# Performance work log

Hardware: AMD Instinct MI355X
Metric: run time of the kernel (lower is better)

Reference implementation:

```python
import jax, jax.numpy as jnp
import numpy as np
import math

B, C_IN, H, W_DIM, D_DIM = 2, 128, 24, 24, 24
D_MODEL, N_HEAD, N_LAYERS, D_FF = 256, 8, 4, 512
D_K = D_MODEL // N_HEAD
EPS = 1e-6


def setup_inputs() -> dict:
    key = jax.random.key(0)
    ks = jax.random.split(key, 16)
    s = 0.02
    inp = {
        "x": jax.random.normal(ks[0], (B, C_IN, H, W_DIM, D_DIM), jnp.float32),
        # 1x1x1 Conv3d W_x: weight [out, in], bias [out]
        "Wx_w": jax.random.normal(ks[1], (D_MODEL, C_IN), jnp.float32) * s,
        "Wx_b": jnp.zeros((D_MODEL,), jnp.float32),
        # per-layer attention projections (stacked over layers)
        "Wq": jax.random.normal(ks[2], (N_LAYERS, D_MODEL, D_MODEL), jnp.float32) * s,
        "bq": jnp.zeros((N_LAYERS, D_MODEL), jnp.float32),
        "Wk": jax.random.normal(ks[3], (N_LAYERS, D_MODEL, D_MODEL), jnp.float32) * s,
        "bk": jnp.zeros((N_LAYERS, D_MODEL), jnp.float32),
        "Wv": jax.random.normal(ks[4], (N_LAYERS, D_MODEL, D_MODEL), jnp.float32) * s,
        "bv": jnp.zeros((N_LAYERS, D_MODEL), jnp.float32),
        "Wo": jax.random.normal(ks[5], (N_LAYERS, D_MODEL, D_MODEL), jnp.float32) * s,
        "bo": jnp.zeros((N_LAYERS, D_MODEL), jnp.float32),
        # layer norms
        "ln1_g": jnp.ones((N_LAYERS, D_MODEL), jnp.float32),
        "ln1_b": jnp.zeros((N_LAYERS, D_MODEL), jnp.float32),
        "ln2_g": jnp.ones((N_LAYERS, D_MODEL), jnp.float32),
        "ln2_b": jnp.zeros((N_LAYERS, D_MODEL), jnp.float32),
        # FFN
        "ffn_w1": jax.random.normal(ks[6], (N_LAYERS, D_MODEL, D_FF), jnp.float32) * s,
        "ffn_b1": jnp.zeros((N_LAYERS, D_FF), jnp.float32),
        "ffn_w2": jax.random.normal(ks[7], (N_LAYERS, D_FF, D_MODEL), jnp.float32) * s,
        "ffn_b2": jnp.zeros((N_LAYERS, D_MODEL), jnp.float32),
        # depthwise 3x3x3 conv positional encoder (groups = D_MODEL)
        "pos_w": jax.random.normal(ks[8], (N_LAYERS, D_MODEL, 1, 3, 3, 3), jnp.float32) * s,
        "pos_b": jnp.zeros((N_LAYERS, D_MODEL), jnp.float32),
    }
    return inp


def _layer_norm(t, g, b):
    mu = jnp.mean(t, axis=-1, keepdims=True)
    var = jnp.var(t, axis=-1, keepdims=True)
    return (t - mu) * jax.lax.rsqrt(var + EPS) * g + b


def reference(x, Wx_w, Wx_b, Wq, bq, Wk, bk, Wv, bv, Wo, bo,
              ln1_g, ln1_b, ln2_g, ln2_b,
              ffn_w1, ffn_b1, ffn_w2, ffn_b2, pos_w, pos_b):
    b = x.shape[0]
    # 1x1x1 conv projection W_x + ReLU (is_up=False path)
    x = jnp.einsum('bchwd,oc->bohwd', x, Wx_w) + Wx_b[None, :, None, None, None]
    x = jax.nn.relu(x)

    inv_sqrt_dk = 1.0 / math.sqrt(D_K)

    for i in range(N_LAYERS):
        # flatten spatial -> tokens: [b, n, d_model]
        t = jnp.transpose(x.reshape(b, D_MODEL, -1), (0, 2, 1))
        n = t.shape[1]

        def heads(y):  # [b,n,d] -> [b,h,n,dk]
            return jnp.transpose(y.reshape(b, n, N_HEAD, D_K), (0, 2, 1, 3))

        q = heads(t @ Wq[i] + bq[i])
        k = heads(t @ Wk[i] + bk[i])
        v = heads(t @ Wv[i] + bv[i])

        # linear attention: softmax over feature dim for q, token dim for k
        q = jax.nn.softmax(q, axis=-1) * inv_sqrt_dk
        k = jax.nn.softmax(k, axis=-2)
        ctx = jnp.einsum('bhnd,bhne->bhde', k, v)     # [b,h,dk,dk]
        o = jnp.einsum('bhnd,bhde->bhne', q, ctx)      # [b,h,n,dk]
        o = jnp.transpose(o, (0, 2, 1, 3)).reshape(b, n, D_MODEL)
        o = o @ Wo[i] + bo[i]

        t = _layer_norm(t + o, ln1_g[i], ln1_b[i])
        f = jax.nn.gelu(t @ ffn_w1[i] + ffn_b1[i], approximate=False) @ ffn_w2[i] + ffn_b2[i]
        t = _layer_norm(t + f, ln2_g[i], ln2_b[i])

        # back to volume and depthwise conv positional embedding
        x = jnp.transpose(t, (0, 2, 1)).reshape(b, D_MODEL, H, W_DIM, D_DIM)
        pos = jax.lax.conv_general_dilated(
            x, pos_w[i], window_strides=(1, 1, 1), padding='SAME',
            dimension_numbers=('NCDHW', 'OIDHW', 'NCDHW'),
            feature_group_count=D_MODEL,
        ) + pos_b[i][None, :, None, None, None]
        x = x + pos
    return x
```

## Files before the change

### kernel.cpp

```cpp
#include <hip/hip_runtime.h>
#include <math.h>

#define NTOK 13824
#define MTOT 27648
#define BATCH 2
#define CIN 128
#define DMODEL 256
#define NHEAD 8
#define NLAYERS 4
#define DFF 512
#define NSPLIT 27
#define KVHALF ((size_t)BATCH * 256 * NTOK)

typedef float f32x4 __attribute__((ext_vector_type(4)));
typedef __bf16 bf16x8 __attribute__((ext_vector_type(8)));
typedef __attribute__((address_space(1))) void gvoid;
typedef __attribute__((address_space(3))) void lvoid;

#define GLDS16(g, l) __builtin_amdgcn_global_load_lds((gvoid*)(g), (lvoid*)(l), 16, 0, 0)

__device__ __forceinline__ unsigned short f2bf(float f) {
    unsigned u = __float_as_uint(f);
    return (unsigned short)((u + 0x7FFFu + ((u >> 16) & 1u)) >> 16);
}
__device__ __forceinline__ float bf2f(unsigned short h) {
    return __uint_as_float(((unsigned)h) << 16);
}

template<int ACT, int OUTM>
__global__ __launch_bounds__(256) void gemm_bf16(
    const unsigned short* __restrict__ A, int lda,
    const unsigned short* __restrict__ Bt, int ldb,
    const float* __restrict__ bias,
    float* __restrict__ Cf, unsigned short* __restrict__ Cb,
    int ldc, int K, long sA, long sB, long sC)
{
    A  += (size_t)blockIdx.z * sA;
    Bt += (size_t)blockIdx.z * sB;
    if (OUTM == 2) Cf += (size_t)blockIdx.z * sC;
    Cb += (size_t)blockIdx.z * sC;

    __shared__ __attribute__((aligned(16))) unsigned short As[4096];
    __shared__ __attribute__((aligned(16))) unsigned short Bs[4096];
    const int t    = threadIdx.x;
    const int lane = t & 63;
    const int wave = t >> 6;
    const int wm = wave & 1, wn = wave >> 1;
    const int m0 = blockIdx.x * 128, n0 = blockIdx.y * 128;

    const int r0   = t >> 2;
    const int koff = (t & 3) * 8;
    const unsigned short* ga0 = A  + (size_t)(m0 + r0)      * lda + koff;
    const unsigned short* ga1 = A  + (size_t)(m0 + r0 + 64) * lda + koff;
    const unsigned short* gb0 = Bt + (size_t)(n0 + r0)      * ldb + koff;
    const unsigned short* gb1 = Bt + (size_t)(n0 + r0 + 64) * ldb + koff;
    unsigned short* la0 = As + t * 8;
    unsigned short* la1 = As + t * 8 + 2048;
    unsigned short* lb0 = Bs + t * 8;
    unsigned short* lb1 = Bs + t * 8 + 2048;

    f32x4 acc[4][4];
    #pragma unroll
    for (int i = 0; i < 4; ++i)
        #pragma unroll
        for (int j = 0; j < 4; ++j) acc[i][j] = (f32x4)0.0f;

    const int fm = lane & 15;
    const int fq = (lane >> 4) * 8;
    const int arow = (wm * 64 + fm) * 32 + fq;
    const int brow = (wn * 64 + fm) * 32 + fq;

    for (int k0 = 0; k0 < K; k0 += 32) {
        GLDS16(ga0 + k0, la0);
        GLDS16(ga1 + k0, la1);
        GLDS16(gb0 + k0, lb0);
        GLDS16(gb1 + k0, lb1);
        __syncthreads();
        bf16x8 af[4], bg[4];
        #pragma unroll
        for (int i = 0; i < 4; ++i) af[i] = *(const bf16x8*)(As + arow + i * 512);
        #pragma unroll
        for (int j = 0; j < 4; ++j) bg[j] = *(const bf16x8*)(Bs + brow + j * 512);
        #pragma unroll
        for (int i = 0; i < 4; ++i)
            #pragma unroll
            for (int j = 0; j < 4; ++j)
                acc[i][j] = __builtin_amdgcn_mfma_f32_16x16x32_bf16(
                    af[i], bg[j], acc[i][j], 0, 0, 0);
        __syncthreads();
    }

    const int cb  = n0 + wn * 64 + fm;
    const int rbs = m0 + wm * 64 + (lane >> 4) * 4;
    #pragma unroll
    for (int j = 0; j < 4; ++j) {
        const int n = cb + j * 16;
        const float bv = bias[n];
        #pragma unroll
        for (int i = 0; i < 4; ++i) {
            #pragma unroll
            for (int r = 0; r < 4; ++r) {
                float v = acc[i][j][r] + bv;
                if (ACT == 1) v = fmaxf(v, 0.0f);
                if (ACT == 2) v = 0.5f * v * (1.0f + erff(v * 0.7071067811865476f));
                const size_t off = (size_t)(rbs + i * 16 + r) * ldc + n;
                if (OUTM == 2) Cf[off] = v;
                Cb[off] = f2bf(v);
            }
        }
    }
}

#define CW_QKV  786432
#define CW_O   1048576
#define CW_1   1572864
#define CW_2   2097152
#define CW_X   2129920
#define CW_B   2132992
__global__ __launch_bounds__(256) void conv_weights(
    const float* __restrict__ Wq, const float* __restrict__ Wk,
    const float* __restrict__ Wv, const float* __restrict__ Wo,
    const float* __restrict__ fw1, const float* __restrict__ fw2,
    const float* __restrict__ Wx_w,
    const float* __restrict__ bq, const float* __restrict__ bk,
    const float* __restrict__ bv,
    unsigned short* __restrict__ wqkv_t, unsigned short* __restrict__ wo_t,
    unsigned short* __restrict__ w1_t, unsigned short* __restrict__ w2_t,
    unsigned short* __restrict__ wx_bf, float* __restrict__ bqkv)
{
    const int e = blockIdx.x * 256 + threadIdx.x;
    if (e < CW_QKV) {
        const int i = e / 196608, r = e % 196608;
        const int n = r / 256, k = r % 256;
        const float* src = (n < 256) ? Wq : (n < 512) ? Wk : Wv;
        wqkv_t[e] = f2bf(src[((size_t)i * 256 + k) * 256 + (n & 255)]);
    } else if (e < CW_O) {
        const int r = e - CW_QKV;
        const int i = r / 65536, rr = r % 65536, n = rr / 256, k = rr % 256;
        wo_t[r] = f2bf(Wo[((size_t)i * 256 + k) * 256 + n]);
    } else if (e < CW_1) {
        const int r = e - CW_O;
        const int i = r / 131072, rr = r % 131072, n = rr / 256, k = rr % 256;
        w1_t[r] = f2bf(fw1[((size_t)i * 256 + k) * 512 + n]);
    } else if (e < CW_2) {
        const int r = e - CW_1;
        const int i = r / 131072, rr = r % 131072, n = rr / 512, k = rr % 512;
        w2_t[r] = f2bf(fw2[((size_t)i * 512 + k) * 256 + n]);
    } else if (e < CW_X) {
        const int r = e - CW_2;
        wx_bf[r] = f2bf(Wx_w[r]);
    } else if (e < CW_B) {
        const int r = e - CW_X;
        const int i = r / 768, j = r % 768;
        const float v = (j < 256) ? bq[i * 256 + j]
                      : (j < 512) ? bk[i * 256 + j - 256]
                                  : bv[i * 256 + j - 512];
        bqkv[r] = v;
    }
}

__global__ __launch_bounds__(256) void conv_x(
    const float* __restrict__ x, unsigned short* __restrict__ xbf)
{
    __shared__ float tile[32][33];
    const int n0 = blockIdx.x * 32;
    const int c0 = blockIdx.y * 32;
    const int b  = blockIdx.z;
    const int t = threadIdx.x;
    const int tn = t & 31, tc = t >> 5;
    #pragma unroll
    for (int p = 0; p < 4; ++p)
        tile[tc + p * 8][tn] =
            x[((size_t)(b * CIN + c0 + tc + p * 8)) * NTOK + n0 + tn];
    __syncthreads();
    const int cc = t & 31, nr = t >> 5;
    #pragma unroll
    for (int p = 0; p < 4; ++p)
        xbf[((size_t)(b * NTOK + n0 + nr + p * 8)) * CIN + c0 + cc] =
            f2bf(tile[cc][nr + p * 8]);
}

__global__ __launch_bounds__(256) void qsm_kernel(unsigned short* __restrict__ qkv)
{
    const int g = blockIdx.x * 256 + threadIdx.x;
    const int row = g >> 5;
    const int cg  = g & 31;
    unsigned short* p = qkv + (size_t)row * 768 + cg * 8;
    uint4 raw = *(const uint4*)p;
    unsigned short* rp = (unsigned short*)&raw;
    float v[8];
    #pragma unroll
    for (int j = 0; j < 8; ++j) v[j] = bf2f(rp[j]);
    float m = v[0];
    #pragma unroll
    for (int j = 1; j < 8; ++j) m = fmaxf(m, v[j]);
    m = fmaxf(m, __shfl_xor(m, 1, 64));
    m = fmaxf(m, __shfl_xor(m, 2, 64));
    float s = 0.0f;
    #pragma unroll
    for (int j = 0; j < 8; ++j) { v[j] = __expf(v[j] - m); s += v[j]; }
    s += __shfl_xor(s, 1, 64);
    s += __shfl_xor(s, 2, 64);
    const float r = 1.0f / s;
    #pragma unroll
    for (int j = 0; j < 8; ++j) rp[j] = f2bf(v[j] * r);
    *(uint4*)p = raw;
}

__global__ __launch_bounds__(256) void kvt_kernel(
    const unsigned short* __restrict__ qkv, unsigned short* __restrict__ kvT)
{
    const int nb = blockIdx.x, h = blockIdx.y, b = blockIdx.z;
    const int n0 = nb * 64;
    const int t = threadIdx.x;
    __shared__ __attribute__((aligned(16))) unsigned short LT[64 * 72];
    const int tl = t >> 2, cg = t & 3;
    const unsigned short* src =
        qkv + ((size_t)(b * NTOK + n0 + tl)) * 768 + 256 + h * 32 + cg * 8;
    const uint4 kr = *(const uint4*)src;
    const uint4 vr = *(const uint4*)(src + 256);
    const unsigned short* ks = (const unsigned short*)&kr;
    const unsigned short* vs = (const unsigned short*)&vr;
    #pragma unroll
    for (int j = 0; j < 8; ++j) {
        const int ch = cg * 8 + j;
        LT[ch * 72 + tl]        = f2bf(__expf(bf2f(ks[j])));
        LT[(32 + ch) * 72 + tl] = vs[j];
    }
    __syncthreads();
    #pragma unroll
    for (int it = 0; it < 2; ++it) {
        const int idx = it * 256 + t;
        const int row = idx >> 3, seg = idx & 7;
        const uint4 val = *(const uint4*)(LT + row * 72 + seg * 8);
        const int ch = row & 31;
        const size_t dst = ((row >= 32) ? KVHALF : (size_t)0)
                         + ((size_t)(b * 256 + h * 32 + ch)) * NTOK + n0 + seg * 8;
        *(uint4*)(kvT + dst) = val;
    }
}

__global__ __launch_bounds__(256) void ctx_mfma(
    const unsigned short* __restrict__ kvT,
    float* __restrict__ ctxp, float* __restrict__ skp)
{
    const int s = blockIdx.x, h = blockIdx.y, b = blockIdx.z;
    const int t = threadIdx.x, w = t >> 6, l = t & 63;
    const int fm = l & 15, fq = (l >> 4) * 8;
    const size_t rowA = (size_t)(b * 256 + h * 32 + fm) * NTOK;
    const int n0 = s * 512 + w * 128 + fq;
    const unsigned short* pa = kvT + rowA + n0;
    const unsigned short* pb = kvT + KVHALF + rowA + n0;

    f32x4 acc[2][2];
    #pragma unroll
    for (int x = 0; x < 2; ++x)
        #pragma unroll
        for (int y = 0; y < 2; ++y) acc[x][y] = (f32x4)0.0f;
    float ss0 = 0.0f, ss1 = 0.0f;

    #pragma unroll
    for (int step = 0; step < 4; ++step) {
        const int ko = step * 32;
        const uint4 ra0 = *(const uint4*)(pa + ko);
        const uint4 ra1 = *(const uint4*)(pa + (size_t)16 * NTOK + ko);
        const uint4 rb0 = *(const uint4*)(pb + ko);
        const uint4 rb1 = *(const uint4*)(pb + (size_t)16 * NTOK + ko);
        const bf16x8 a0 = *(const bf16x8*)&ra0;
        const bf16x8 a1 = *(const bf16x8*)&ra1;
        const bf16x8 b0 = *(const bf16x8*)&rb0;
        const bf16x8 b1 = *(const bf16x8*)&rb1;
        acc[0][0] = __builtin_amdgcn_mfma_f32_16x16x32_bf16(a0, b0, acc[0][0], 0, 0, 0);
        acc[0][1] = __builtin_amdgcn_mfma_f32_16x16x32_bf16(a0, b1, acc[0][1], 0, 0, 0);
        acc[1][0] = __builtin_amdgcn_mfma_f32_16x16x32_bf16(a1, b0, acc[1][0], 0, 0, 0);
        acc[1][1] = __builtin_amdgcn_mfma_f32_16x16x32_bf16(a1, b1, acc[1][1], 0, 0, 0);
        const unsigned short* u0 = (const unsigned short*)&ra0;
        const unsigned short* u1 = (const unsigned short*)&ra1;
        #pragma unroll
        for (int j = 0; j < 8; ++j) { ss0 += bf2f(u0[j]); ss1 += bf2f(u1[j]); }
    }

    ss0 += __shfl_xor(ss0, 16, 64); ss0 += __shfl_xor(ss0, 32, 64);
    ss1 += __shfl_xor(ss1, 16, 64); ss1 += __shfl_xor(ss1, 32, 64);
    __shared__ float skw[4][32];
    __shared__ float redc[4][32][33];
    if (l < 16) { skw[w][fm] = ss0; skw[w][16 + fm] = ss1; }

    const int rb4 = (l >> 4) * 4;
    #pragma unroll
    for (int x = 0; x < 2; ++x)
        #pragma unroll
        for (int y = 0; y < 2; ++y)
            #pragma unroll
            for (int r = 0; r < 4; ++r)
                redc[w][x * 16 + rb4 + r][y * 16 + fm] = acc[x][y][r];
    __syncthreads();

    if (t < 32)
        skp[(size_t)s * 512 + b * 256 + h * 32 + t] =
            skw[0][t] + skw[1][t] + skw[2][t] + skw[3][t];

    const int e0 = t * 4;
    const int dd = e0 >> 5, c0 = e0 & 31;
    float4 o;
    o.x = redc[0][dd][c0+0] + redc[1][dd][c0+0] + redc[2][dd][c0+0] + redc[3][dd][c0+0];
    o.y = redc[0][dd][c0+1] + redc[1][dd][c0+1] + redc[2][dd][c0+1] + redc[3][dd][c0+1];
    o.z = redc[0][dd][c0+2] + redc[1][dd][c0+2] + redc[2][dd][c0+2] + redc[3][dd][c0+2];
    o.w = redc[0][dd][c0+3] + redc[1][dd][c0+3] + redc[2][dd][c0+3] + redc[3][dd][c0+3];
    *(float4*)(ctxp + ((size_t)s * 16 + b * 8 + h) * 1024 + e0) = o;
}

__global__ __launch_bounds__(256) void ctxred(
    const float* __restrict__ ctxp, const float* __restrict__ skp,
    float* __restrict__ ctx, float* __restrict__ Sk)
{
    const int o = blockIdx.x * 256 + threadIdx.x;
    if (o < 16384) {
        float a = 0.0f;
        for (int s = 0; s < NSPLIT; ++s) a += ctxp[(size_t)s * 16384 + o];
        ctx[o] = a;
    } else {
        const int c = o - 16384;
        float a = 0.0f;
        for (int s = 0; s < NSPLIT; ++s) a += skp[(size_t)s * 512 + c];
        Sk[c] = a;
    }
}

__global__ __launch_bounds__(256) void ctxwo_kernel(
    const float* __restrict__ ctx, const float* __restrict__ Sk,
    const unsigned short* __restrict__ wo_t, unsigned short* __restrict__ wp)
{
    const int h = blockIdx.x, b = blockIdx.y;
    const int n = threadIdx.x;
    __shared__ float cl[1024];
    __shared__ float sdk[32];
    {
        const float* cp = ctx + (size_t)(b * 8 + h) * 1024;
        *(float4*)&cl[n * 4] = *(const float4*)&cp[n * 4];
    }
    if (n < 32) sdk[n] = 0.17677669529663687f / Sk[b * 256 + h * 32 + n];
    __syncthreads();
    float w[32];
    const unsigned short* wop = wo_t + (size_t)n * 256 + h * 32;
    #pragma unroll
    for (int e = 0; e < 32; ++e) w[e] = bf2f(wop[e]);
    unsigned short outv[32];
    #pragma unroll
    for (int d = 0; d < 32; ++d) {
        float acc = 0.0f;
        #pragma unroll
        for (int e = 0; e < 32; ++e) acc += cl[d * 32 + e] * w[e];
        outv[d] = f2bf(acc * sdk[d]);
    }
    unsigned short* op = wp + (size_t)b * 65536 + (size_t)n * 256 + h * 32;
    #pragma unroll
    for (int d = 0; d < 32; d += 8)
        *(uint4*)(op + d) = *(uint4*)(outv + d);
}

template<int WB>
__global__ __launch_bounds__(256) void ln_kernel(
    float* __restrict__ t, const unsigned short* __restrict__ add,
    const float* __restrict__ g, const float* __restrict__ bta,
    unsigned short* __restrict__ tbf)
{
    const int row = blockIdx.x;
    const int c = threadIdx.x;
    const int lane = c & 63, wave = c >> 6;
    const size_t off = (size_t)row * 256 + c;
    const float v = t[off] + bf2f(add[off]);
    __shared__ float red[8];
    float s = v;
    #pragma unroll
    for (int o = 32; o; o >>= 1) s += __shfl_xor(s, o, 64);
    if (lane == 0) red[wave] = s;
    __syncthreads();
    const float mu = (red[0] + red[1] + red[2] + red[3]) * (1.0f / 256.0f);
    const float dv = v - mu;
    float s2 = dv * dv;
    #pragma unroll
    for (int o = 32; o; o >>= 1) s2 += __shfl_xor(s2, o, 64);
    if (lane == 0) red[wave + 4] = s2;
    __syncthreads();
    const float var = (red[4] + red[5] + red[6] + red[7]) * (1.0f / 256.0f);
    const float o = dv * rsqrtf(var + 1e-6f) * g[c] + bta[c];
    t[off] = o;
    if (WB) tbf[off] = f2bf(o);
}

template<int WB>
__global__ __launch_bounds__(256) void posconv_kernel(
    const float* __restrict__ tin, const float* __restrict__ pw,
    const float* __restrict__ pb, float* __restrict__ outp,
    unsigned short* __restrict__ tbfp)
{
    const int hw = blockIdx.x;
    const int b  = blockIdx.y;
    const int hh = hw / 24, ww = hw % 24;
    const int c  = threadIdx.x;

    float w[27];
    #pragma unroll
    for (int k = 0; k < 27; ++k) w[k] = pw[c * 27 + k];
    const float bias = pb[c];

    const float* base = tin + (size_t)b * NTOK * 256 + c;

    const float* colp[9];
    bool colok[9];
    #pragma unroll
    for (int dh = -1; dh <= 1; ++dh)
        #pragma unroll
        for (int dw = -1; dw <= 1; ++dw) {
            const int j = (dh + 1) * 3 + (dw + 1);
            const int h2 = hh + dh, w2 = ww + dw;
            colok[j] = ((unsigned)h2 < 24u) & ((unsigned)w2 < 24u);
            colp[j] = base + (size_t)((h2 * 24 + w2) * 24) * 256;
        }

    float win[9][3];
    #pragma unroll
    for (int j = 0; j < 9; ++j) {
        win[j][0] = 0.0f;
        win[j][1] = colok[j] ? colp[j][0] : 0.0f;
    }

    float* ob = outp + ((size_t)b * NTOK + (size_t)hw * 24) * 256 + c;
    unsigned short* tb = WB ? (tbfp + ((size_t)b * NTOK + (size_t)hw * 24) * 256 + c)
                            : (unsigned short*)nullptr;

    for (int d = 0; d < 24; ++d) {
        #pragma unroll
        for (int j = 0; j < 9; ++j)
            win[j][2] = (colok[j] && d < 23) ? colp[j][(d + 1) * 256] : 0.0f;

        float acc = bias + win[4][1];
        #pragma unroll
        for (int j = 0; j < 9; ++j) {
            acc += w[j * 3 + 0] * win[j][0];
            acc += w[j * 3 + 1] * win[j][1];
            acc += w[j * 3 + 2] * win[j][2];
        }
        ob[d * 256] = acc;
        if (WB) tb[d * 256] = f2bf(acc);

        #pragma unroll
        for (int j = 0; j < 9; ++j) { win[j][0] = win[j][1]; win[j][1] = win[j][2]; }
    }
}

__global__ __launch_bounds__(256) void tr_out(
    const float* __restrict__ tin, float* __restrict__ outp)
{
    __shared__ float tile[32][33];
    const int m0 = blockIdx.x * 32;
    const int c0 = blockIdx.y * 32;
    const int t = threadIdx.x;
    const int tc = t & 31, tr = t >> 5;
    #pragma unroll
    for (int r = 0; r < 4; ++r)
        tile[tr + r * 8][tc] = tin[(size_t)(m0 + tr + r * 8) * 256 + c0 + tc];
    __syncthreads();
    const int b = (m0 >= NTOK) ? 1 : 0;
    const int n0 = m0 - b * NTOK;
    #pragma unroll
    for (int r = 0; r < 4; ++r)
        outp[((size_t)b * 256 + c0 + tr + r * 8) * NTOK + n0 + tc] = tile[tc][tr + r * 8];
}

extern "C" void kernel_launch(void* const* d_in, const int* in_sizes, int n_in,
                              void* d_out, int out_size, void* d_ws, size_t ws_size,
                              hipStream_t stream)
{
    (void)in_sizes; (void)n_in; (void)out_size; (void)ws_size;
    const float* x     = (const float*)d_in[0];
    const float* Wx_w  = (const float*)d_in[1];
    const float* Wx_b  = (const float*)d_in[2];
    const float* Wq    = (const float*)d_in[3];
    const float* bq    = (const float*)d_in[4];
    const float* Wk    = (const float*)d_in[5];
    const float* bk    = (const float*)d_in[6];
    const float* Wv    = (const float*)d_in[7];
    const float* bv    = (const float*)d_in[8];
    const float* Wo    = (const float*)d_in[9];
    const float* bo    = (const float*)d_in[10];
    const float* ln1_g = (const float*)d_in[11];
    const float* ln1_b = (const float*)d_in[12];
    const float* ln2_g = (const float*)d_in[13];
    const float* ln2_b = (const float*)d_in[14];
    const float* fw1   = (const float*)d_in[15];
    const float* fb1   = (const float*)d_in[16];
    const float* fw2   = (const float*)d_in[17];
    const float* fb2   = (const float*)d_in[18];
    const float* pw    = (const float*)d_in[19];
    const float* pb    = (const float*)d_in[20];
    float* out = (float*)d_out;

    char* p = (char*)d_ws;
    float* tA            = (float*)p;          p += (size_t)MTOT * 256 * 4;
    float* tB            = (float*)p;          p += (size_t)MTOT * 256 * 4;
    unsigned short* tbf  = (unsigned short*)p; p += (size_t)MTOT * 256 * 2;
    unsigned short* qkv  = (unsigned short*)p; p += (size_t)MTOT * 768 * 2;
    unsigned short* hbf  = (unsigned short*)p; p += (size_t)MTOT * 512 * 2;
    unsigned short* ob   = (unsigned short*)p; p += (size_t)MTOT * 256 * 2;
    unsigned short* xbf  = (unsigned short*)p; p += (size_t)MTOT * 128 * 2;
    unsigned short* wqkv_t = (unsigned short*)p; p += (size_t)786432 * 2;
    unsigned short* wo_t   = (unsigned short*)p; p += (size_t)262144 * 2;
    unsigned short* w1_t   = (unsigned short*)p; p += (size_t)524288 * 2;
    unsigned short* w2_t   = (unsigned short*)p; p += (size_t)524288 * 2;
    unsigned short* wx_bf  = (unsigned short*)p; p += (size_t)32768 * 2;
    unsigned short* wp     = (unsigned short*)p; p += (size_t)BATCH * 65536 * 2;
    float* bqkv = (float*)p; p += 3072 * 4;
    float* ctx  = (float*)p; p += 16384 * 4;
    float* Sk   = (float*)p; p += 512 * 4;
    float* ctxp = (float*)p; p += (size_t)NSPLIT * 16384 * 4;
    float* skp  = (float*)p; p += (size_t)NSPLIT * 512 * 4;
    unsigned short* kvT = hbf;

    hipLaunchKernelGGL(conv_weights, dim3(8333), dim3(256), 0, stream,
                       Wq, Wk, Wv, Wo, fw1, fw2, Wx_w, bq, bk, bv,
                       wqkv_t, wo_t, w1_t, w2_t, wx_bf, bqkv);
    hipLaunchKernelGGL(conv_x, dim3(NTOK / 32, CIN / 32, BATCH), dim3(256), 0, stream,
                       x, xbf);

    hipLaunchKernelGGL((gemm_bf16<1, 2>), dim3(216, 2, 1), dim3(256), 0, stream,
                       xbf, CIN, wx_bf, CIN, Wx_b, tA, tbf, 256, CIN,
                       (long)0, (long)0, (long)0);

    for (int i = 0; i < NLAYERS; ++i) {
        float* tin  = (i & 1) ? tB : tA;
        float* tout = (i & 1) ? tA : tB;

        hipLaunchKernelGGL((gemm_bf16<0, 1>), dim3(216, 6, 1), dim3(256), 0, stream,
                           tbf, 256, wqkv_t + (size_t)i * 196608, 256,
                           bqkv + i * 768, nullptr, qkv, 768, 256,
                           (long)0, (long)0, (long)0);

        hipLaunchKernelGGL(kvt_kernel, dim3(NTOK / 64, NHEAD, BATCH), dim3(256), 0, stream,
                           qkv, kvT);
        hipLaunchKernelGGL(ctx_mfma, dim3(NSPLIT, NHEAD, BATCH), dim3(256), 0, stream,
                           kvT, ctxp, skp);
        hipLaunchKernelGGL(ctxred, dim3(66), dim3(256), 0, stream, ctxp, skp, ctx, Sk);

        hipLaunchKernelGGL(qsm_kernel, dim3(3456), dim3(256), 0, stream, qkv);
        hipLaunchKernelGGL(ctxwo_kernel, dim3(NHEAD, BATCH), dim3(256), 0, stream,
                           ctx, Sk, wo_t + (size_t)i * 65536, wp);

        hipLaunchKernelGGL((gemm_bf16<0, 1>), dim3(108, 2, BATCH), dim3(256), 0, stream,
                           qkv, 768, wp, 256, bo + i * 256, nullptr, ob, 256, 256,
                           (long)NTOK * 768, (long)65536, (long)NTOK * 256);

        hipLaunchKernelGGL((ln_kernel<1>), dim3(MTOT), dim3(256), 0, stream,
                           tin, ob, ln1_g + i * 256, ln1_b + i * 256, tbf);

        hipLaunchKernelGGL((gemm_bf16<2, 1>), dim3(216, 4, 1), dim3(256), 0, stream,
                           tbf, 256, w1_t + (size_t)i * 131072, 256,
                           fb1 + i * 512, nullptr, hbf, 512, 256,
                           (long)0, (long)0, (long)0);
        hipLaunchKernelGGL((gemm_bf16<0, 1>), dim3(216, 2, 1), dim3(256), 0, stream,
                           hbf, 512, w2_t + (size_t)i * 131072, 512,
                           fb2 + i * 256, nullptr, ob, 256, 512,
                           (long)0, (long)0, (long)0);
        hipLaunchKernelGGL((ln_kernel<0>), dim3(MTOT), dim3(256), 0, stream,
                           tin, ob, ln2_g + i * 256, ln2_b + i * 256, nullptr);

        if (i < NLAYERS - 1)
            hipLaunchKernelGGL((posconv_kernel<1>), dim3(576, BATCH), dim3(256), 0, stream,
                               tin, pw + (size_t)i * 6912, pb + i * 256, tout, tbf);
        else
            hipLaunchKernelGGL((posconv_kernel<0>), dim3(576, BATCH), dim3(256), 0, stream,
                               tin, pw + (size_t)i * 6912, pb + i * 256, tout, nullptr);
    }

    hipLaunchKernelGGL(tr_out, dim3(MTOT / 32, 8), dim3(256), 0, stream, tA, out);
}
```

Measured before the change: 903.4 us.

## Prepack GEMM weights in MFMA fragment order and load operands directly to registers

Weights, including the per-batch ctx·Wo product, are now stored pre-swizzled in MFMA B-fragment order, so each lane reads its fragment from global memory with one contiguous 16-byte load. The GEMM no longer stages tiles through LDS, has no barriers, takes K and LDA as template parameters so the K loop fully unrolls, and remaps blocks across the eight XCDs. The batched output-projection GEMM becomes a 2D grid that picks its weight slice per M-tile. The risk is that A-operand reads straight from global memory are strided and uncoalesced, and nothing is double-buffered to hide their latency.

```diff
diff --git a/kernel.cpp b/kernel.cpp
--- a/kernel.cpp
+++ b/kernel.cpp
@@ -14,10 +14,6 @@
 
 typedef float f32x4 __attribute__((ext_vector_type(4)));
 typedef __bf16 bf16x8 __attribute__((ext_vector_type(8)));
-typedef __attribute__((address_space(1))) void gvoid;
-typedef __attribute__((address_space(3))) void lvoid;
-
-#define GLDS16(g, l) __builtin_amdgcn_global_load_lds((gvoid*)(g), (lvoid*)(l), 16, 0, 0)
 
 __device__ __forceinline__ unsigned short f2bf(float f) {
     unsigned u = __float_as_uint(f);
@@ -27,37 +23,45 @@
     return __uint_as_float(((unsigned)h) << 16);
 }
 
-template<int ACT, int OUTM>
+__device__ __forceinline__ void fragpos(int d, int kdiv32, int& n, int& k) {
+    const int e = d & 7, l = (d >> 3) & 63, blk = d >> 9;
+    const int ks = blk % kdiv32, nt = blk / kdiv32;
+    n = nt * 16 + (l & 15);
+    k = ks * 32 + ((l >> 4) << 3) + e;
+}
+
+template<int ACT, int OUTM, int K, int LDA>
 __global__ __launch_bounds__(256) void gemm_bf16(
-    const unsigned short* __restrict__ A, int lda,
-    const unsigned short* __restrict__ Bt, int ldb,
+    const unsigned short* __restrict__ A,
+    const unsigned short* __restrict__ Bf,
     const float* __restrict__ bias,
     float* __restrict__ Cf, unsigned short* __restrict__ Cb,
-    int ldc, int K, long sA, long sB, long sC)
-{
-    A  += (size_t)blockIdx.z * sA;
-    Bt += (size_t)blockIdx.z * sB;
-    if (OUTM == 2) Cf += (size_t)blockIdx.z * sC;
-    Cb += (size_t)blockIdx.z * sC;
-
-    __shared__ __attribute__((aligned(16))) unsigned short As[4096];
-    __shared__ __attribute__((aligned(16))) unsigned short Bs[4096];
+    int ldc, int mtb, long sB, int swz)
+{
+    constexpr int KS = K / 32;
+
+    int bx = blockIdx.x, by = blockIdx.y;
+    if (swz) {
+        const int nx  = gridDim.x;
+        const int lin = by * nx + bx;
+        const int mpx = nx >> 3;
+        const int xcd = lin & 7, loc = lin >> 3;
+        bx = xcd * mpx + loc % mpx;
+        by = loc / mpx;
+    }
+    Bf += (size_t)(bx / mtb) * sB;
+
     const int t    = threadIdx.x;
     const int lane = t & 63;
     const int wave = t >> 6;
     const int wm = wave & 1, wn = wave >> 1;
-    const int m0 = blockIdx.x * 128, n0 = blockIdx.y * 128;
-
-    const int r0   = t >> 2;
-    const int koff = (t & 3) * 8;
-    const unsigned short* ga0 = A  + (size_t)(m0 + r0)      * lda + koff;
-    const unsigned short* ga1 = A  + (size_t)(m0 + r0 + 64) * lda + koff;
-    const unsigned short* gb0 = Bt + (size_t)(n0 + r0)      * ldb + koff;
-    const unsigned short* gb1 = Bt + (size_t)(n0 + r0 + 64) * ldb + koff;
-    unsigned short* la0 = As + t * 8;
-    unsigned short* la1 = As + t * 8 + 2048;
-    unsigned short* lb0 = Bs + t * 8;
-    unsigned short* lb1 = Bs + t * 8 + 2048;
+    const int m0 = bx * 128, n0 = by * 128;
+    const int fm  = lane & 15;
+    const int fq8 = (lane >> 4) * 8;
+
+    const unsigned short* pa = A + (size_t)(m0 + wm * 64 + fm) * LDA + fq8;
+    const unsigned short* pb =
+        Bf + (size_t)((n0 >> 4) + wn * 4) * KS * 512 + lane * 8;
 
     f32x4 acc[4][4];
     #pragma unroll
@@ -65,29 +69,21 @@
         #pragma unroll
         for (int j = 0; j < 4; ++j) acc[i][j] = (f32x4)0.0f;
 
-    const int fm = lane & 15;
-    const int fq = (lane >> 4) * 8;
-    const int arow = (wm * 64 + fm) * 32 + fq;
-    const int brow = (wn * 64 + fm) * 32 + fq;
-
-    for (int k0 = 0; k0 < K; k0 += 32) {
-        GLDS16(ga0 + k0, la0);
-        GLDS16(ga1 + k0, la1);
-        GLDS16(gb0 + k0, lb0);
-        GLDS16(gb1 + k0, lb1);
-        __syncthreads();
+    #pragma unroll
+    for (int ks = 0; ks < KS; ++ks) {
         bf16x8 af[4], bg[4];
         #pragma unroll
-        for (int i = 0; i < 4; ++i) af[i] = *(const bf16x8*)(As + arow + i * 512);
-        #pragma unroll
-        for (int j = 0; j < 4; ++j) bg[j] = *(const bf16x8*)(Bs + brow + j * 512);
+        for (int i = 0; i < 4; ++i)
+            af[i] = *(const bf16x8*)(pa + (size_t)i * 16 * LDA + ks * 32);
+        #pragma unroll
+        for (int j = 0; j < 4; ++j)
+            bg[j] = *(const bf16x8*)(pb + ((size_t)j * KS + ks) * 512);
         #pragma unroll
         for (int i = 0; i < 4; ++i)
             #pragma unroll
             for (int j = 0; j < 4; ++j)
                 acc[i][j] = __builtin_amdgcn_mfma_f32_16x16x32_bf16(
                     af[i], bg[j], acc[i][j], 0, 0, 0);
-        __syncthreads();
     }
 
     const int cb  = n0 + wn * 64 + fm;
@@ -130,8 +126,8 @@
 {
     const int e = blockIdx.x * 256 + threadIdx.x;
     if (e < CW_QKV) {
-        const int i = e / 196608, r = e % 196608;
-        const int n = r / 256, k = r % 256;
+        const int i = e / 196608, d = e % 196608;
+        int n, k; fragpos(d, 8, n, k);
         const float* src = (n < 256) ? Wq : (n < 512) ? Wk : Wv;
         wqkv_t[e] = f2bf(src[((size_t)i * 256 + k) * 256 + (n & 255)]);
     } else if (e < CW_O) {
@@ -140,15 +136,18 @@
         wo_t[r] = f2bf(Wo[((size_t)i * 256 + k) * 256 + n]);
     } else if (e < CW_1) {
         const int r = e - CW_O;
-        const int i = r / 131072, rr = r % 131072, n = rr / 256, k = rr % 256;
+        const int i = r / 131072, d = r % 131072;
+        int n, k; fragpos(d, 8, n, k);
         w1_t[r] = f2bf(fw1[((size_t)i * 256 + k) * 512 + n]);
     } else if (e < CW_2) {
         const int r = e - CW_1;
-        const int i = r / 131072, rr = r % 131072, n = rr / 512, k = rr % 512;
+        const int i = r / 131072, d = r % 131072;
+        int n, k; fragpos(d, 16, n, k);
         w2_t[r] = f2bf(fw2[((size_t)i * 512 + k) * 256 + n]);
     } else if (e < CW_X) {
-        const int r = e - CW_2;
-        wx_bf[r] = f2bf(Wx_w[r]);
+        const int d = e - CW_2;
+        int n, k; fragpos(d, 4, n, k);
+        wx_bf[d] = f2bf(Wx_w[n * 128 + k]);
     } else if (e < CW_B) {
         const int r = e - CW_X;
         const int i = r / 768, j = r % 768;
@@ -353,10 +352,11 @@
         for (int e = 0; e < 32; ++e) acc += cl[d * 32 + e] * w[e];
         outv[d] = f2bf(acc * sdk[d]);
     }
-    unsigned short* op = wp + (size_t)b * 65536 + (size_t)n * 256 + h * 32;
-    #pragma unroll
-    for (int d = 0; d < 32; d += 8)
-        *(uint4*)(op + d) = *(uint4*)(outv + d);
+    unsigned short* op = wp + (size_t)b * 65536
+                       + ((size_t)((n >> 4) * 8 + h)) * 512 + (n & 15) * 8;
+    #pragma unroll
+    for (int d8 = 0; d8 < 4; ++d8)
+        *(uint4*)(op + d8 * 128) = *(uint4*)(outv + d8 * 8);
 }
 
 template<int WB>
@@ -518,24 +518,24 @@
     float* skp  = (float*)p; p += (size_t)NSPLIT * 512 * 4;
     unsigned short* kvT = hbf;
 
+    const int BIG = 1 << 30;
+
     hipLaunchKernelGGL(conv_weights, dim3(8333), dim3(256), 0, stream,
                        Wq, Wk, Wv, Wo, fw1, fw2, Wx_w, bq, bk, bv,
                        wqkv_t, wo_t, w1_t, w2_t, wx_bf, bqkv);
     hipLaunchKernelGGL(conv_x, dim3(NTOK / 32, CIN / 32, BATCH), dim3(256), 0, stream,
                        x, xbf);
 
-    hipLaunchKernelGGL((gemm_bf16<1, 2>), dim3(216, 2, 1), dim3(256), 0, stream,
-                       xbf, CIN, wx_bf, CIN, Wx_b, tA, tbf, 256, CIN,
-                       (long)0, (long)0, (long)0);
+    hipLaunchKernelGGL((gemm_bf16<1, 2, 128, 128>), dim3(216, 2), dim3(256), 0, stream,
+                       xbf, wx_bf, Wx_b, tA, tbf, 256, BIG, (long)0, 1);
 
     for (int i = 0; i < NLAYERS; ++i) {
         float* tin  = (i & 1) ? tB : tA;
         float* tout = (i & 1) ? tA : tB;
 
-        hipLaunchKernelGGL((gemm_bf16<0, 1>), dim3(216, 6, 1), dim3(256), 0, stream,
-                           tbf, 256, wqkv_t + (size_t)i * 196608, 256,
-                           bqkv + i * 768, nullptr, qkv, 768, 256,
-                           (long)0, (long)0, (long)0);
+        hipLaunchKernelGGL((gemm_bf16<0, 1, 256, 256>), dim3(216, 6), dim3(256), 0, stream,
+                           tbf, wqkv_t + (size_t)i * 196608,
+                           bqkv + i * 768, nullptr, qkv, 768, BIG, (long)0, 1);
 
         hipLaunchKernelGGL(kvt_kernel, dim3(NTOK / 64, NHEAD, BATCH), dim3(256), 0, stream,
                            qkv, kvT);
@@ -547,21 +547,19 @@
         hipLaunchKernelGGL(ctxwo_kernel, dim3(NHEAD, BATCH), dim3(256), 0, stream,
                            ctx, Sk, wo_t + (size_t)i * 65536, wp);
 
-        hipLaunchKernelGGL((gemm_bf16<0, 1>), dim3(108, 2, BATCH), dim3(256), 0, stream,
-                           qkv, 768, wp, 256, bo + i * 256, nullptr, ob, 256, 256,
-                           (long)NTOK * 768, (long)65536, (long)NTOK * 256);
+        hipLaunchKernelGGL((gemm_bf16<0, 1, 256, 768>), dim3(216, 2), dim3(256), 0, stream,
+                           qkv, wp, bo + i * 256, nullptr, ob, 256,
+                           108, (long)65536, 1);
 
         hipLaunchKernelGGL((ln_kernel<1>), dim3(MTOT), dim3(256), 0, stream,
                            tin, ob, ln1_g + i * 256, ln1_b + i * 256, tbf);
 
-        hipLaunchKernelGGL((gemm_bf16<2, 1>), dim3(216, 4, 1), dim3(256), 0, stream,
-                           tbf, 256, w1_t + (size_t)i * 131072, 256,
-                           fb1 + i * 512, nullptr, hbf, 512, 256,
-                           (long)0, (long)0, (long)0);
-        hipLaunchKernelGGL((gemm_bf16<0, 1>), dim3(216, 2, 1), dim3(256), 0, stream,
-                           hbf, 512, w2_t + (size_t)i * 131072, 512,
-                           fb2 + i * 256, nullptr, ob, 256, 512,
-                           (long)0, (long)0, (long)0);
+        hipLaunchKernelGGL((gemm_bf16<2, 1, 256, 256>), dim3(216, 4), dim3(256), 0, stream,
+                           tbf, w1_t + (size_t)i * 131072,
+                           fb1 + i * 512, nullptr, hbf, 512, BIG, (long)0, 1);
+        hipLaunchKernelGGL((gemm_bf16<0, 1, 512, 512>), dim3(216, 2), dim3(256), 0, stream,
+                           hbf, w2_t + (size_t)i * 131072,
+                           fb2 + i * 256, nullptr, ob, 256, BIG, (long)0, 1);
         hipLaunchKernelGGL((ln_kernel<0>), dim3(MTOT), dim3(256), 0, stream,
                            tin, ob, ln2_g + i * 256, ln2_b + i * 256, nullptr);
 
```

New measurement: 991.2 us. +9.7%, slower.

## Double-buffer GEMM LDS tiles with K=64 steps and XOR-swizzled layout

Applied to the files above, without the earlier changes.

The bf16 MFMA GEMM now stages 64-wide K tiles into two LDS buffers. It issues the async global-to-LDS loads for the next tile before computing on the current one, which halves barriers per K and overlaps memory with MFMA work. An XOR swizzle on the column index is meant to avoid LDS bank conflicts on fragment reads. LDS use grows fourfold to 64KB per block, which may reduce occupancy, and K must be a multiple of 64.

```diff
diff --git a/kernel.cpp b/kernel.cpp
--- a/kernel.cpp
+++ b/kernel.cpp
@@ -40,24 +40,18 @@
     if (OUTM == 2) Cf += (size_t)blockIdx.z * sC;
     Cb += (size_t)blockIdx.z * sC;
 
-    __shared__ __attribute__((aligned(16))) unsigned short As[4096];
-    __shared__ __attribute__((aligned(16))) unsigned short Bs[4096];
+    __shared__ __attribute__((aligned(16))) unsigned short As[2][8192];
+    __shared__ __attribute__((aligned(16))) unsigned short Bs[2][8192];
     const int t    = threadIdx.x;
     const int lane = t & 63;
     const int wave = t >> 6;
     const int wm = wave & 1, wn = wave >> 1;
     const int m0 = blockIdx.x * 128, n0 = blockIdx.y * 128;
 
-    const int r0   = t >> 2;
-    const int koff = (t & 3) * 8;
-    const unsigned short* ga0 = A  + (size_t)(m0 + r0)      * lda + koff;
-    const unsigned short* ga1 = A  + (size_t)(m0 + r0 + 64) * lda + koff;
-    const unsigned short* gb0 = Bt + (size_t)(n0 + r0)      * ldb + koff;
-    const unsigned short* gb1 = Bt + (size_t)(n0 + r0 + 64) * ldb + koff;
-    unsigned short* la0 = As + t * 8;
-    unsigned short* la1 = As + t * 8 + 2048;
-    unsigned short* lb0 = Bs + t * 8;
-    unsigned short* lb1 = Bs + t * 8 + 2048;
+    const int srow = t >> 3;
+    const int skid = ((t & 7) * 8) ^ ((srow & 7) << 3);
+    const unsigned short* ga = A  + (size_t)(m0 + srow) * lda + skid;
+    const unsigned short* gb = Bt + (size_t)(n0 + srow) * ldb + skid;
 
     f32x4 acc[4][4];
     #pragma unroll
@@ -65,30 +59,56 @@
         #pragma unroll
         for (int j = 0; j < 4; ++j) acc[i][j] = (f32x4)0.0f;
 
-    const int fm = lane & 15;
-    const int fq = (lane >> 4) * 8;
-    const int arow = (wm * 64 + fm) * 32 + fq;
-    const int brow = (wn * 64 + fm) * 32 + fq;
-
-    for (int k0 = 0; k0 < K; k0 += 32) {
-        GLDS16(ga0 + k0, la0);
-        GLDS16(ga1 + k0, la1);
-        GLDS16(gb0 + k0, lb0);
-        GLDS16(gb1 + k0, lb1);
+    const int fm  = lane & 15;
+    const int fq8 = (lane >> 4) * 8;
+    const int sw3 = (fm & 7) << 3;
+    const int arow = (wm * 64 + fm) * 64;
+    const int brow = (wn * 64 + fm) * 64;
+
+#define STAGE(bufi, kk)                                                        \
+    {                                                                          \
+        _Pragma("unroll")                                                      \
+        for (int p = 0; p < 4; ++p) {                                          \
+            GLDS16(ga + (size_t)p * 32 * lda + (kk), &As[bufi][p * 2048 + t * 8]); \
+            GLDS16(gb + (size_t)p * 32 * ldb + (kk), &Bs[bufi][p * 2048 + t * 8]); \
+        }                                                                      \
+    }
+
+#define COMPUTE(bufi)                                                          \
+    {                                                                          \
+        _Pragma("unroll")                                                      \
+        for (int ks = 0; ks < 2; ++ks) {                                       \
+            bf16x8 af[4], bg[4];                                               \
+            const int kidx = (fq8 + ks * 32) ^ sw3;                            \
+            _Pragma("unroll")                                                  \
+            for (int i = 0; i < 4; ++i)                                        \
+                af[i] = *(const bf16x8*)(&As[bufi][arow + i * 1024 + kidx]);   \
+            _Pragma("unroll")                                                  \
+            for (int j = 0; j < 4; ++j)                                        \
+                bg[j] = *(const bf16x8*)(&Bs[bufi][brow + j * 1024 + kidx]);   \
+            _Pragma("unroll")                                                  \
+            for (int i = 0; i < 4; ++i)                                        \
+                _Pragma("unroll")                                              \
+                for (int j = 0; j < 4; ++j)                                    \
+                    acc[i][j] = __builtin_amdgcn_mfma_f32_16x16x32_bf16(       \
+                        af[i], bg[j], acc[i][j], 0, 0, 0);                     \
+        }                                                                      \
+    }
+
+    STAGE(0, 0)
+    __syncthreads();
+    const int NT = K >> 6;
+    int cur = 0;
+    for (int t64 = 0; t64 < NT - 1; ++t64) {
+        STAGE(cur ^ 1, (t64 + 1) * 64)
+        COMPUTE(cur)
         __syncthreads();
-        bf16x8 af[4], bg[4];
-        #pragma unroll
-        for (int i = 0; i < 4; ++i) af[i] = *(const bf16x8*)(As + arow + i * 512);
-        #pragma unroll
-        for (int j = 0; j < 4; ++j) bg[j] = *(const bf16x8*)(Bs + brow + j * 512);
-        #pragma unroll
-        for (int i = 0; i < 4; ++i)
-            #pragma unroll
-            for (int j = 0; j < 4; ++j)
-                acc[i][j] = __builtin_amdgcn_mfma_f32_16x16x32_bf16(
-                    af[i], bg[j], acc[i][j], 0, 0, 0);
-        __syncthreads();
-    }
+        cur ^= 1;
+    }
+    COMPUTE(cur)
+
+#undef STAGE
+#undef COMPUTE
 
     const int cb  = n0 + wn * 64 + fm;
     const int rbs = m0 + wm * 64 + (lane >> 4) * 4;
```

Measured after the change: 866.8 us. 1.04x faster.

## Stage full-K GEMM tiles in swizzled LDS and reuse B tile across M blocks

Applied to the files above, without the earlier changes.

The bf16 GEMM now makes K a compile-time template parameter and loads up to 256 columns of K into LDS per stage, instead of looping over 32-wide K slices with two barriers each. The LDS layout gets an XOR swizzle to avoid bank conflicts on the MFMA fragment reads. A new G parameter lets one block keep its B tile resident and walk several consecutive M tiles, overlapping the next A load with the epilogue. This cuts barrier count and B reloads, but uses 128 KB of LDS per block at KT=256, which lowers occupancy and leaves little latency hiding beyond that one overlap.

```diff
diff --git a/kernel.cpp b/kernel.cpp
--- a/kernel.cpp
+++ b/kernel.cpp
@@ -27,87 +27,131 @@
     return __uint_as_float(((unsigned)h) << 16);
 }
 
-template<int ACT, int OUTM>
+template<int ACT, int OUTM, int K, int G>
 __global__ __launch_bounds__(256) void gemm_bf16(
     const unsigned short* __restrict__ A, int lda,
     const unsigned short* __restrict__ Bt, int ldb,
     const float* __restrict__ bias,
     float* __restrict__ Cf, unsigned short* __restrict__ Cb,
-    int ldc, int K, long sA, long sB, long sC)
-{
+    int ldc, long sA, long sB, long sC)
+{
+    constexpr int KT  = (K < 256) ? K : 256;
+    constexpr int NKC = K / KT;
+    constexpr int KSN = KT / 32;
+    constexpr int CPR = KT / 8;
+    constexpr int RPP = 256 / CPR;
+    constexpr int NP  = 128 / RPP;
+
     A  += (size_t)blockIdx.z * sA;
     Bt += (size_t)blockIdx.z * sB;
     if (OUTM == 2) Cf += (size_t)blockIdx.z * sC;
     Cb += (size_t)blockIdx.z * sC;
 
-    __shared__ __attribute__((aligned(16))) unsigned short As[4096];
-    __shared__ __attribute__((aligned(16))) unsigned short Bs[4096];
+    __shared__ __attribute__((aligned(16))) unsigned short As[128 * KT];
+    __shared__ __attribute__((aligned(16))) unsigned short Bs[128 * KT];
+
     const int t    = threadIdx.x;
     const int lane = t & 63;
     const int wave = t >> 6;
     const int wm = wave & 1, wn = wave >> 1;
-    const int m0 = blockIdx.x * 128, n0 = blockIdx.y * 128;
-
-    const int r0   = t >> 2;
-    const int koff = (t & 3) * 8;
-    const unsigned short* ga0 = A  + (size_t)(m0 + r0)      * lda + koff;
-    const unsigned short* ga1 = A  + (size_t)(m0 + r0 + 64) * lda + koff;
-    const unsigned short* gb0 = Bt + (size_t)(n0 + r0)      * ldb + koff;
-    const unsigned short* gb1 = Bt + (size_t)(n0 + r0 + 64) * ldb + koff;
-    unsigned short* la0 = As + t * 8;
-    unsigned short* la1 = As + t * 8 + 2048;
-    unsigned short* lb0 = Bs + t * 8;
-    unsigned short* lb1 = Bs + t * 8 + 2048;
+    const int n0 = blockIdx.y * 128;
+
+    const int srow = t / CPR;
+    const int sk   = ((t % CPR) * 8) ^ ((srow & 7) << 3);
+
+    const int fm  = lane & 15;
+    const int fq8 = (lane >> 4) * 8;
+    const int sw3 = (fm & 7) << 3;
 
     f32x4 acc[4][4];
-    #pragma unroll
-    for (int i = 0; i < 4; ++i)
-        #pragma unroll
-        for (int j = 0; j < 4; ++j) acc[i][j] = (f32x4)0.0f;
-
-    const int fm = lane & 15;
-    const int fq = (lane >> 4) * 8;
-    const int arow = (wm * 64 + fm) * 32 + fq;
-    const int brow = (wn * 64 + fm) * 32 + fq;
-
-    for (int k0 = 0; k0 < K; k0 += 32) {
-        GLDS16(ga0 + k0, la0);
-        GLDS16(ga1 + k0, la1);
-        GLDS16(gb0 + k0, lb0);
-        GLDS16(gb1 + k0, lb1);
+
+    auto STAGE_A = [&](int m0, int kc) {
+        #pragma unroll
+        for (int p = 0; p < NP; ++p)
+            GLDS16(A + (size_t)(m0 + p * RPP + srow) * lda + kc * KT + sk,
+                   &As[p * 2048 + t * 8]);
+    };
+    auto STAGE_B = [&](int kc) {
+        #pragma unroll
+        for (int p = 0; p < NP; ++p)
+            GLDS16(Bt + (size_t)(n0 + p * RPP + srow) * ldb + kc * KT + sk,
+                   &Bs[p * 2048 + t * 8]);
+    };
+    auto COMPUTE = [&]() {
+        #pragma unroll
+        for (int ks = 0; ks < KSN; ++ks) {
+            bf16x8 af[4], bg[4];
+            const int kidx = (ks * 32 + fq8) ^ sw3;
+            #pragma unroll
+            for (int i = 0; i < 4; ++i)
+                af[i] = *(const bf16x8*)(&As[(wm * 64 + i * 16 + fm) * KT + kidx]);
+            #pragma unroll
+            for (int j = 0; j < 4; ++j)
+                bg[j] = *(const bf16x8*)(&Bs[(wn * 64 + j * 16 + fm) * KT + kidx]);
+            #pragma unroll
+            for (int i = 0; i < 4; ++i)
+                #pragma unroll
+                for (int j = 0; j < 4; ++j)
+                    acc[i][j] = __builtin_amdgcn_mfma_f32_16x16x32_bf16(
+                        af[i], bg[j], acc[i][j], 0, 0, 0);
+        }
+    };
+    auto EPILOGUE = [&](int m0) {
+        const int cb  = n0 + wn * 64 + fm;
+        const int rbs = m0 + wm * 64 + (lane >> 4) * 4;
+        #pragma unroll
+        for (int j = 0; j < 4; ++j) {
+            const int n = cb + j * 16;
+            const float bv = bias[n];
+            #pragma unroll
+            for (int i = 0; i < 4; ++i) {
+                #pragma unroll
+                for (int r = 0; r < 4; ++r) {
+                    float v = acc[i][j][r] + bv;
+                    if (ACT == 1) v = fmaxf(v, 0.0f);
+                    if (ACT == 2) v = 0.5f * v * (1.0f + erff(v * 0.7071067811865476f));
+                    const size_t off = (size_t)(rbs + i * 16 + r) * ldc + n;
+                    if (OUTM == 2) Cf[off] = v;
+                    Cb[off] = f2bf(v);
+                }
+            }
+        }
+    };
+
+    if constexpr (NKC == 1) {
+        const int mb0 = blockIdx.x * (G * 128);
+        STAGE_A(mb0, 0);
+        STAGE_B(0);
         __syncthreads();
-        bf16x8 af[4], bg[4];
-        #pragma unroll
-        for (int i = 0; i < 4; ++i) af[i] = *(const bf16x8*)(As + arow + i * 512);
-        #pragma unroll
-        for (int j = 0; j < 4; ++j) bg[j] = *(const bf16x8*)(Bs + brow + j * 512);
+        #pragma unroll
+        for (int g = 0; g < G; ++g) {
+            #pragma unroll
+            for (int i = 0; i < 4; ++i)
+                #pragma unroll
+                for (int j = 0; j < 4; ++j) acc[i][j] = (f32x4)0.0f;
+            COMPUTE();
+            if (g + 1 < G) {
+                __syncthreads();
+                STAGE_A(mb0 + (g + 1) * 128, 0);
+            }
+            EPILOGUE(mb0 + g * 128);
+            if (g + 1 < G) __syncthreads();
+        }
+    } else {
+        const int m0 = blockIdx.x * 128;
         #pragma unroll
         for (int i = 0; i < 4; ++i)
             #pragma unroll
-            for (int j = 0; j < 4; ++j)
-                acc[i][j] = __builtin_amdgcn_mfma_f32_16x16x32_bf16(
-                    af[i], bg[j], acc[i][j], 0, 0, 0);
-        __syncthreads();
-    }
-
-    const int cb  = n0 + wn * 64 + fm;
-    const int rbs = m0 + wm * 64 + (lane >> 4) * 4;
-    #pragma unroll
-    for (int j = 0; j < 4; ++j) {
-        const int n = cb + j * 16;
-        const float bv = bias[n];
-        #pragma unroll
-        for (int i = 0; i < 4; ++i) {
-            #pragma unroll
-            for (int r = 0; r < 4; ++r) {
-                float v = acc[i][j][r] + bv;
-                if (ACT == 1) v = fmaxf(v, 0.0f);
-                if (ACT == 2) v = 0.5f * v * (1.0f + erff(v * 0.7071067811865476f));
-                const size_t off = (size_t)(rbs + i * 16 + r) * ldc + n;
-                if (OUTM == 2) Cf[off] = v;
-                Cb[off] = f2bf(v);
-            }
+            for (int j = 0; j < 4; ++j) acc[i][j] = (f32x4)0.0f;
+        #pragma unroll
+        for (int kc = 0; kc < NKC; ++kc) {
+            if (kc) __syncthreads();
+            STAGE_A(m0, kc);
+            STAGE_B(kc);
+            __syncthreads();
+            COMPUTE();
         }
+        EPILOGUE(m0);
     }
 }
 
@@ -524,17 +568,17 @@
     hipLaunchKernelGGL(conv_x, dim3(NTOK / 32, CIN / 32, BATCH), dim3(256), 0, stream,
                        x, xbf);
 
-    hipLaunchKernelGGL((gemm_bf16<1, 2>), dim3(216, 2, 1), dim3(256), 0, stream,
-                       xbf, CIN, wx_bf, CIN, Wx_b, tA, tbf, 256, CIN,
+    hipLaunchKernelGGL((gemm_bf16<1, 2, 128, 1>), dim3(216, 2, 1), dim3(256), 0, stream,
+                       xbf, CIN, wx_bf, CIN, Wx_b, tA, tbf, 256,
                        (long)0, (long)0, (long)0);
 
     for (int i = 0; i < NLAYERS; ++i) {
         float* tin  = (i & 1) ? tB : tA;
         float* tout = (i & 1) ? tA : tB;
 
-        hipLaunchKernelGGL((gemm_bf16<0, 1>), dim3(216, 6, 1), dim3(256), 0, stream,
+        hipLaunchKernelGGL((gemm_bf16<0, 1, 256, 3>), dim3(72, 6, 1), dim3(256), 0, stream,
                            tbf, 256, wqkv_t + (size_t)i * 196608, 256,
-                           bqkv + i * 768, nullptr, qkv, 768, 256,
+                           bqkv + i * 768, nullptr, qkv, 768,
                            (long)0, (long)0, (long)0);
 
         hipLaunchKernelGGL(kvt_kernel, dim3(NTOK / 64, NHEAD, BATCH), dim3(256), 0, stream,
@@ -547,20 +591,20 @@
         hipLaunchKernelGGL(ctxwo_kernel, dim3(NHEAD, BATCH), dim3(256), 0, stream,
                            ctx, Sk, wo_t + (size_t)i * 65536, wp);
 
-        hipLaunchKernelGGL((gemm_bf16<0, 1>), dim3(108, 2, BATCH), dim3(256), 0, stream,
-                           qkv, 768, wp, 256, bo + i * 256, nullptr, ob, 256, 256,
+        hipLaunchKernelGGL((gemm_bf16<0, 1, 256, 1>), dim3(108, 2, BATCH), dim3(256), 0, stream,
+                           qkv, 768, wp, 256, bo + i * 256, nullptr, ob, 256,
                            (long)NTOK * 768, (long)65536, (long)NTOK * 256);
 
         hipLaunchKernelGGL((ln_kernel<1>), dim3(MTOT), dim3(256), 0, stream,
                            tin, ob, ln1_g + i * 256, ln1_b + i * 256, tbf);
 
-        hipLaunchKernelGGL((gemm_bf16<2, 1>), dim3(216, 4, 1), dim3(256), 0, stream,
+        hipLaunchKernelGGL((gemm_bf16<2, 1, 256, 2>), dim3(108, 4, 1), dim3(256), 0, stream,
                            tbf, 256, w1_t + (size_t)i * 131072, 256,
-                           fb1 + i * 512, nullptr, hbf, 512, 256,
+                           fb1 + i * 512, nullptr, hbf, 512,
                            (long)0, (long)0, (long)0);
-        hipLaunchKernelGGL((gemm_bf16<0, 1>), dim3(216, 2, 1), dim3(256), 0, stream,
+        hipLaunchKernelGGL((gemm_bf16<0, 1, 512, 1>), dim3(216, 2, 1), dim3(256), 0, stream,
                            hbf, 512, w2_t + (size_t)i * 131072, 512,
-                           fb2 + i * 256, nullptr, ob, 256, 512,
+                           fb2 + i * 256, nullptr, ob, 256,
                            (long)0, (long)0, (long)0);
         hipLaunchKernelGGL((ln_kernel<0>), dim3(MTOT), dim3(256), 0, stream,
                            tin, ob, ln2_g + i * 256, ln2_b + i * 256, nullptr);
```

Result: slower. 975.5 us (+8.0%).
